# Kernel optimization log

Hardware: AMD Instinct MI355X
Metric: run time of the kernel (lower is better)

Reference implementation:

```python
import jax, jax.numpy as jnp
import numpy as np

BETA = 0.5        # membrane decay (from source)
THRESHOLD = 1.0   # snn.Leaky default
ALPHA = 2.0       # ATan surrogate default slope (snntorch)


@jax.custom_vjp
def spike_fn(v):
    # Heaviside spike: 1 where membrane - threshold > 0
    return (v > 0).astype(v.dtype)


def _spike_fwd(v):
    return spike_fn(v), v


def _spike_bwd(v, g):
    # snntorch ATan surrogate gradient: (alpha/2) / (1 + (pi/2*alpha*v)^2)
    grad = (ALPHA / 2.0) / (1.0 + (jnp.pi / 2.0 * ALPHA * v) ** 2)
    return (g * grad,)


spike_fn.defvjp(_spike_fwd, _spike_bwd)


def setup_inputs() -> dict:
    key = jax.random.key(0)
    # x: [T, B, N] = [num_steps, batch, neurons]
    x = jax.random.normal(key, (128, 64, 4096), dtype=jnp.float32)
    return {"x": x}


def reference(x):
    # snntorch Leaky with init_hidden=True, reset_mechanism='subtract':
    #   reset_t = H(mem_{t-1} - thr)
    #   mem_t   = beta*mem_{t-1} + x_t - reset_t*thr
    #   spk_t   = H(mem_t - thr)
    mem0 = jnp.zeros(x.shape[1:], dtype=x.dtype)

    def step(mem, xt):
        reset = spike_fn(mem - THRESHOLD)
        mem_new = BETA * mem + xt - reset * THRESHOLD
        spk = spike_fn(mem_new - THRESHOLD)
        return mem_new, spk

    _, spk_rec = jax.lax.scan(step, mem0, x)  # spk_rec: [T, B, N]
    return spk_rec
```

## Files before the change

kernel.cpp:

```cpp
#include <hip/hip_runtime.h>


#define T_STEPS 128
#define T_HALF 64
#define D 8

__device__ __forceinline__ float4 lif_step(float4& mem, const float4 v) {
    mem.x = 0.5f * mem.x + v.x - (mem.x > 1.0f ? 1.0f : 0.0f);
    mem.y = 0.5f * mem.y + v.y - (mem.y > 1.0f ? 1.0f : 0.0f);
    mem.z = 0.5f * mem.z + v.z - (mem.z > 1.0f ? 1.0f : 0.0f);
    mem.w = 0.5f * mem.w + v.w - (mem.w > 1.0f ? 1.0f : 0.0f);
    float4 s;
    s.x = mem.x > 1.0f ? 1.0f : 0.0f;
    s.y = mem.y > 1.0f ? 1.0f : 0.0f;
    s.z = mem.z > 1.0f ? 1.0f : 0.0f;
    s.w = mem.w > 1.0f ? 1.0f : 0.0f;
    return s;
}

__global__ __launch_bounds__(256) void snn_leaky_fwd(const float4* __restrict__ x,
                                                     float4* __restrict__ out,
                                                     int n4) {
    const int chunk = blockIdx.x & 255;
    const int phase = blockIdx.x >> 8;
    const int col = chunk * 256 + threadIdx.x;

    const float4* xp = x + col;
    float4* op = out + col;

    float4 buf[D];
    float4 mem = make_float4(0.f, 0.f, 0.f, 0.f);

#pragma unroll
    for (int u = 0; u < D; ++u) buf[u] = xp[(size_t)u * n4];

    if (phase == 0) {
#pragma unroll
        for (int t = 0; t < T_HALF; ++t) {
            const float4 v = buf[t % D];
            if (t + D < T_HALF) buf[t % D] = xp[(size_t)(t + D) * n4];
            const float4 s = lif_step(mem, v);
            op[(size_t)t * n4] = s;
        }
    } else {
#pragma unroll
        for (int t = 0; t < T_HALF; ++t) {
            const float4 v = buf[t % D];
            buf[t % D] = xp[(size_t)(t + D) * n4];
            (void)lif_step(mem, v);
        }
#pragma unroll
        for (int t = T_HALF; t < T_STEPS; ++t) {
            const float4 v = buf[t % D];
            if (t + D < T_STEPS) buf[t % D] = xp[(size_t)(t + D) * n4];
            const float4 s = lif_step(mem, v);
            op[(size_t)t * n4] = s;
        }
    }
}

extern "C" void kernel_launch(void* const* d_in, const int* in_sizes, int n_in,
                              void* d_out, int out_size, void* d_ws, size_t ws_size,
                              hipStream_t stream) {
    const float4* x = (const float4*)d_in[0];
    float4* out = (float4*)d_out;

    const int total = in_sizes[0];
    const int n4 = total / T_STEPS / 4;

    snn_leaky_fwd<<<512, 256, 0, stream>>>(x, out, n4);
}
```

Measured before the change: 226.2 us.

## Split time axis into four redundant-prefix phases with 1024-thread blocks

Generalizes the two-phase time split to four phases. Each block recomputes the membrane recurrence from t=0 up to the end of its segment but writes only its own quarter of the outputs. Blocks grow to 1024 threads, giving 256 blocks. This shortens the critical path of the longest block, at the cost of more redundant input reads (roughly 1+2+3+4 quarters of x) and a rolled outer loop with runtime branches.

```diff
diff --git a/kernel.cpp b/kernel.cpp
--- a/kernel.cpp
+++ b/kernel.cpp
@@ -2,7 +2,8 @@
 
 
 #define T_STEPS 128
-#define T_HALF 64
+#define PHASES 4
+#define ACTIVE (T_STEPS / PHASES)
 #define D 8
 
 __device__ __forceinline__ float4 lif_step(float4& mem, const float4 v) {
@@ -18,15 +19,18 @@
     return s;
 }
 
-__global__ __launch_bounds__(256) void snn_leaky_fwd(const float4* __restrict__ x,
-                                                     float4* __restrict__ out,
-                                                     int n4) {
-    const int chunk = blockIdx.x & 255;
-    const int phase = blockIdx.x >> 8;
-    const int col = chunk * 256 + threadIdx.x;
+__global__ __launch_bounds__(1024) void snn_leaky_fwd(const float4* __restrict__ x,
+                                                      float4* __restrict__ out,
+                                                      int n4) {
+    const int chunk = blockIdx.x & 63;
+    const int phase = blockIdx.x >> 6;
+    const int col = chunk * 1024 + threadIdx.x;
 
     const float4* xp = x + col;
     float4* op = out + col;
+
+    const int s = phase * ACTIVE;
+    const int tEnd = s + ACTIVE;
 
     float4 buf[D];
     float4 mem = make_float4(0.f, 0.f, 0.f, 0.f);
@@ -34,27 +38,15 @@
 #pragma unroll
     for (int u = 0; u < D; ++u) buf[u] = xp[(size_t)u * n4];
 
-    if (phase == 0) {
+    for (int tb = 0; tb < tEnd; tb += D) {
+        const bool active = (tb >= s);
 #pragma unroll
-        for (int t = 0; t < T_HALF; ++t) {
-            const float4 v = buf[t % D];
-            if (t + D < T_HALF) buf[t % D] = xp[(size_t)(t + D) * n4];
-            const float4 s = lif_step(mem, v);
-            op[(size_t)t * n4] = s;
-        }
-    } else {
-#pragma unroll
-        for (int t = 0; t < T_HALF; ++t) {
-            const float4 v = buf[t % D];
-            buf[t % D] = xp[(size_t)(t + D) * n4];
-            (void)lif_step(mem, v);
-        }
-#pragma unroll
-        for (int t = T_HALF; t < T_STEPS; ++t) {
-            const float4 v = buf[t % D];
-            if (t + D < T_STEPS) buf[t % D] = xp[(size_t)(t + D) * n4];
-            const float4 s = lif_step(mem, v);
-            op[(size_t)t * n4] = s;
+        for (int u = 0; u < D; ++u) {
+            const int t = tb + u;
+            const float4 v = buf[u];
+            if (t + D < tEnd) buf[u] = xp[(size_t)(t + D) * n4];
+            const float4 spk = lif_step(mem, v);
+            if (active) op[(size_t)t * n4] = spk;
         }
     }
 }
@@ -68,5 +60,5 @@
     const int total = in_sizes[0];
     const int n4 = total / T_STEPS / 4;
 
-    snn_leaky_fwd<<<512, 256, 0, stream>>>(x, out, n4);
+    snn_leaky_fwd<<<PHASES * 64, 1024, 0, stream>>>(x, out, n4);
 }
```

New measurement: 243.4 us. 1.08x slower.
